# Optimization experiments

Measured on AMD Instinct MI355X. Metric: run time of the kernel, lower is better.

## Reference

```python
import jax, jax.numpy as jnp
import numpy as np


def setup_inputs() -> dict:
    key = jax.random.key(0)
    x = jax.random.normal(key, (4, 256, 64, 64), dtype=jnp.float32)
    return {"x": x}


def reference(x):
    # x: [B, C, W, H]
    B, C, W, H = x.shape
    N = W * H
    q = x.reshape(B, C, N).transpose(0, 2, 1)  # [B, N, C] (proj_query)
    # per-token L2 norm over channels
    q_norm = jnp.linalg.norm(q, ord=2, axis=2)  # [B, N]
    # outer product of norms: [B, N, N]
    nm = q_norm[:, :, None] * q_norm[:, None, :]
    # raw dot-product energy: [B, N, N]
    energy = jnp.einsum('bnc,bmc->bnm', q, q)
    norm_energy = energy / (nm + 1e-6)
    attention = jax.nn.softmax(norm_energy, axis=-1)
    return attention
```

## Files before the change

kernel.cpp:

```cpp
#include <hip/hip_runtime.h>
#include <hip/hip_bf16.h>

#define BATCH 4
#define CDIM  256
#define NTOK  4096

#define BM 64
#define BN 256

typedef short bf16x8 __attribute__((ext_vector_type(8)));
typedef float floatx4 __attribute__((ext_vector_type(4)));
typedef unsigned int uintx4 __attribute__((ext_vector_type(4)));
typedef unsigned int u32;

#define PIN(v) asm volatile("" : "+v"(v))
#define WAIT(n) asm volatile("s_waitcnt vmcnt(" #n ")" ::: "memory")
#define LGKM0() asm volatile("s_waitcnt lgkmcnt(0)" ::: "memory")
#define BAR() do { __builtin_amdgcn_s_barrier(); asm volatile("" ::: "memory"); } while (0)

__device__ inline u32 f2bf1(float f) {
    u32 u = __float_as_uint(f);
    u += 0x7fffu + ((u >> 16) & 1u);
    return u >> 16;
}
__device__ inline u32 f2bf2(float lo, float hi) { return f2bf1(lo) | (f2bf1(hi) << 16); }

__device__ inline void gload_lds16(const short* g, short* l) {
    __builtin_amdgcn_global_load_lds(
        (const __attribute__((address_space(1))) u32*)g,
        (__attribute__((address_space(3))) u32*)l, 16, 0, 0);
}

#define TT 32
__global__ __launch_bounds__(256) void prep_kernel(const float* __restrict__ x,
                                                   short* __restrict__ xn) {
    __shared__ float tile[TT][CDIM + 2];
    __shared__ float part[8][TT];
    __shared__ float rinv_s[TT];
    const int tid = threadIdx.x;
    const int blk = blockIdx.x;
    const int b = blk >> 7;
    const int t0 = (blk & 127) * TT;
    const float* xb = x + (size_t)b * CDIM * NTOK;
    const int ti = tid & 31, cq = tid >> 5;
    float ss = 0.f;
    for (int c = cq; c < CDIM; c += 8) {
        float v = xb[(size_t)c * NTOK + t0 + ti];
        tile[ti][c] = v;
        ss += v * v;
    }
    part[cq][ti] = ss;
    __syncthreads();
    if (tid < TT) {
        float s = 0.f;
#pragma unroll
        for (int q = 0; q < 8; ++q) s += part[q][tid];
        rinv_s[tid] = 1.0f / sqrtf(s);
    }
    __syncthreads();
    const int tok = tid >> 3, seg = tid & 7;
    const float ri = rinv_s[tok];
    size_t obase = ((size_t)(b * NTOK + t0 + tok)) * CDIM + seg * 32;
#pragma unroll
    for (int j = 0; j < 4; ++j) {
        u32 w[4];
#pragma unroll
        for (int u = 0; u < 4; ++u) {
            float f0 = tile[tok][seg * 32 + j * 8 + 2 * u] * ri;
            float f1 = tile[tok][seg * 32 + j * 8 + 2 * u + 1] * ri;
            w[u] = f2bf2(f0, f1);
        }
        *(uintx4*)&xn[obase + j * 8] = (uintx4){w[0], w[1], w[2], w[3]};
    }
}

__global__ __launch_bounds__(512, 2) void attn_kernel(const short* __restrict__ xn,
                                                      float* __restrict__ out) {
    __shared__ short Bs[4][256][64];
    __shared__ float rowsumLds[BM][8];
    const int tid = threadIdx.x;
    const int D = blockIdx.x;
    const int L = ((D & 7) << 5) + (D >> 3);
    const int b = L >> 6;
    const int rb = (L & 63) * BM;
    const short* xnb = xn + (size_t)b * NTOK * CDIM;
    float* outb = out + ((size_t)b << 24);
    const int lane = tid & 63, wid = tid >> 6;
    const int wcol = wid << 5;
    const int r0 = lane & 15, kq = lane >> 4;
    const int sx = r0 & 7;
    const int tr0 = wcol + r0, tr1 = wcol + 16 + r0;

    const int trl = (wid << 3) + (lane >> 3);
    const int c8 = (lane & 7) ^ (lane >> 3);

    bf16x8 afr[4][8];
#pragma unroll
    for (int m = 0; m < 4; ++m) {
        const short* arow = xnb + (size_t)(rb + m * 16 + r0) * CDIM;
#pragma unroll
        for (int j = 0; j < 8; ++j) {
            afr[m][j] = *(const bf16x8*)(arow + j * 32 + kq * 8);
            PIN(afr[m][j]);
        }
    }

    float psum[16];
#pragma unroll
    for (int i = 0; i < 16; ++i) psum[i] = 0.f;
    floatx4 acc[4][2];
    bf16x8 nb00, nb10, nb01, nb11;

    auto stage = [&](int ct, int kc) {
        const short* s0 = xnb + (size_t)(ct * BN + trl) * CDIM + kc * 64 + c8 * 8;
        short* d = &Bs[kc][wid << 3][0];
#pragma unroll
        for (int rr = 0; rr < 4; ++rr)
            gload_lds16(s0 + (size_t)(rr * 64) * CDIM, d + rr * 64 * 64);
    };

#define ACCZERO() do { _Pragma("unroll") for (int m = 0; m < 4; ++m) { \
        acc[m][0] = (floatx4){0,0,0,0}; acc[m][1] = (floatx4){0,0,0,0}; } } while (0)

#define DSREAD(KC) do { \
    const int p0 = kq ^ sx, p1 = (4 | kq) ^ sx; \
    nb00 = *(const bf16x8*)&Bs[KC][tr0][p0 * 8]; \
    nb10 = *(const bf16x8*)&Bs[KC][tr1][p0 * 8]; \
    nb01 = *(const bf16x8*)&Bs[KC][tr0][p1 * 8]; \
    nb11 = *(const bf16x8*)&Bs[KC][tr1][p1 * 8]; \
} while (0)

#define MFMA16(KC) do { \
    LGKM0(); \
    __builtin_amdgcn_sched_barrier(0); \
    __builtin_amdgcn_s_setprio(1); \
    _Pragma("unroll") for (int m = 0; m < 4; ++m) \
        acc[m][0] = __builtin_amdgcn_mfma_f32_16x16x32_bf16(afr[m][(KC)*2], nb00, acc[m][0], 0,0,0); \
    _Pragma("unroll") for (int m = 0; m < 4; ++m) \
        acc[m][1] = __builtin_amdgcn_mfma_f32_16x16x32_bf16(afr[m][(KC)*2], nb10, acc[m][1], 0,0,0); \
    _Pragma("unroll") for (int m = 0; m < 4; ++m) \
        acc[m][0] = __builtin_amdgcn_mfma_f32_16x16x32_bf16(afr[m][(KC)*2+1], nb01, acc[m][0], 0,0,0); \
    _Pragma("unroll") for (int m = 0; m < 4; ++m) \
        acc[m][1] = __builtin_amdgcn_mfma_f32_16x16x32_bf16(afr[m][(KC)*2+1], nb11, acc[m][1], 0,0,0); \
    __builtin_amdgcn_s_setprio(0); \
} while (0)

#define EPI0() do { \
    _Pragma("unroll") for (int m = 0; m < 4; ++m) \
    _Pragma("unroll") for (int r = 0; r < 4; ++r) \
        psum[m * 4 + r] += __expf(acc[m][0][r] - 1.f) + __expf(acc[m][1][r] - 1.f); \
} while (0)

#define EPI1(CT) do { \
    _Pragma("unroll") for (int m = 0; m < 4; ++m) \
    _Pragma("unroll") for (int r = 0; r < 4; ++r) { \
        const int row = rb + m * 16 + kq * 4 + r; \
        float* p = outb + ((size_t)row << 12) + ((CT) << 8) + wcol + r0; \
        const float ri = psum[m * 4 + r]; \
        __builtin_nontemporal_store(__expf(acc[m][0][r] - 1.f) * ri, p); \
        __builtin_nontemporal_store(__expf(acc[m][1][r] - 1.f) * ri, p + 16); } \
} while (0)

    stage(0, 0); stage(0, 1);
    WAIT(4); BAR();
    DSREAD(0); stage(0, 2);
    WAIT(4); BAR();
    ACCZERO();
    for (int ct = 0; ct < 15; ++ct) {
        MFMA16(0); stage(ct, 3);     WAIT(4); DSREAD(1); BAR();
        MFMA16(1); stage(ct + 1, 0); WAIT(4); DSREAD(2); BAR();
        MFMA16(2); stage(ct + 1, 1); WAIT(4); DSREAD(3); BAR();
        MFMA16(3); EPI0(); ACCZERO(); stage(ct + 1, 2); WAIT(4); DSREAD(0); BAR();
    }
    MFMA16(0); stage(15, 3); WAIT(4); DSREAD(1); BAR();
    MFMA16(1); WAIT(0); DSREAD(2); BAR();
    MFMA16(2); DSREAD(3); BAR();
    MFMA16(3); EPI0();

#pragma unroll
    for (int m = 0; m < 4; ++m)
#pragma unroll
        for (int r = 0; r < 4; ++r) {
            float v = psum[m * 4 + r];
            v += __shfl_xor(v, 1); v += __shfl_xor(v, 2);
            v += __shfl_xor(v, 4); v += __shfl_xor(v, 8);
            if (r0 == 0) rowsumLds[m * 16 + kq * 4 + r][wid] = v;
        }
    __syncthreads();
#pragma unroll
    for (int m = 0; m < 4; ++m)
#pragma unroll
        for (int r = 0; r < 4; ++r) {
            const int row = m * 16 + kq * 4 + r;
            float s = 0.f;
#pragma unroll
            for (int w = 0; w < 8; ++w) s += rowsumLds[row][w];
            psum[m * 4 + r] = 1.0f / s;
        }
    __syncthreads();

    stage(0, 0); stage(0, 1);
    WAIT(4); BAR();
    DSREAD(0); stage(0, 2);
    WAIT(4); BAR();
    ACCZERO();
    {
        MFMA16(0); stage(0, 3); WAIT(4); DSREAD(1); BAR();
        MFMA16(1); stage(1, 0); WAIT(4); DSREAD(2); BAR();
        MFMA16(2); stage(1, 1); WAIT(4); DSREAD(3); BAR();
        MFMA16(3); stage(1, 2); EPI1(0); ACCZERO(); WAIT(36); DSREAD(0); BAR();
    }
    for (int ct = 1; ct < 15; ++ct) {
        MFMA16(0); stage(ct, 3);     WAIT(36); DSREAD(1); BAR();
        MFMA16(1); stage(ct + 1, 0); WAIT(4);  DSREAD(2); BAR();
        MFMA16(2); stage(ct + 1, 1); WAIT(4);  DSREAD(3); BAR();
        MFMA16(3); stage(ct + 1, 2); EPI1(ct); ACCZERO(); WAIT(36); DSREAD(0); BAR();
    }
    MFMA16(0); stage(15, 3); WAIT(36); DSREAD(1); BAR();
    MFMA16(1); WAIT(0); DSREAD(2); BAR();
    MFMA16(2); DSREAD(3); BAR();
    MFMA16(3); EPI1(15);

#undef ACCZERO
#undef DSREAD
#undef MFMA16
#undef EPI0
#undef EPI1
}

extern "C" void kernel_launch(void* const* d_in, const int* in_sizes, int n_in,
                              void* d_out, int out_size, void* d_ws, size_t ws_size,
                              hipStream_t stream) {
    const float* x = (const float*)d_in[0];
    float* out = (float*)d_out;
    short* xn = (short*)d_ws;

    prep_kernel<<<BATCH * (NTOK / TT), 256, 0, stream>>>(x, xn);
    attn_kernel<<<NTOK / BM * BATCH, 512, 0, stream>>>(xn, out);
}
```

Before: 155.7 us.

## Split attention block across 16 waves with 2x8 warp grid

Doubles the attention kernel's block to 1024 threads and arranges the 16 waves as a 2x8 grid, so each wave now covers 32 rows instead of 64. This halves per-wave A fragments, accumulators and MFMA count, and halves per-thread staging loads. The wait counts are retuned to match, and in the second pass the epilogue stores move after the next LDS read. The aim is more waves per block to hide latency and lower register pressure. In exchange, B-tile reuse per wave drops (the MFMA-to-LDS-read ratio halves) and block-wide barriers now synchronize twice as many waves.

```diff
diff --git a/kernel.cpp b/kernel.cpp
--- a/kernel.cpp
+++ b/kernel.cpp
@@ -74,8 +74,8 @@
     }
 }
 
-__global__ __launch_bounds__(512, 2) void attn_kernel(const short* __restrict__ xn,
-                                                      float* __restrict__ out) {
+__global__ __launch_bounds__(1024) void attn_kernel(const short* __restrict__ xn,
+                                                    float* __restrict__ out) {
     __shared__ short Bs[4][256][64];
     __shared__ float rowsumLds[BM][8];
     const int tid = threadIdx.x;
@@ -86,18 +86,19 @@
     const short* xnb = xn + (size_t)b * NTOK * CDIM;
     float* outb = out + ((size_t)b << 24);
     const int lane = tid & 63, wid = tid >> 6;
-    const int wcol = wid << 5;
+    const int wr = (wid >> 3) << 5;
+    const int wcol = (wid & 7) << 5;
     const int r0 = lane & 15, kq = lane >> 4;
     const int sx = r0 & 7;
     const int tr0 = wcol + r0, tr1 = wcol + 16 + r0;
 
-    const int trl = (wid << 3) + (lane >> 3);
-    const int c8 = (lane & 7) ^ (lane >> 3);
-
-    bf16x8 afr[4][8];
-#pragma unroll
-    for (int m = 0; m < 4; ++m) {
-        const short* arow = xnb + (size_t)(rb + m * 16 + r0) * CDIM;
+    const int trl = tid >> 3;
+    const int c8 = (tid & 7) ^ (trl & 7);
+
+    bf16x8 afr[2][8];
+#pragma unroll
+    for (int m = 0; m < 2; ++m) {
+        const short* arow = xnb + (size_t)(rb + wr + m * 16 + r0) * CDIM;
 #pragma unroll
         for (int j = 0; j < 8; ++j) {
             afr[m][j] = *(const bf16x8*)(arow + j * 32 + kq * 8);
@@ -105,21 +106,20 @@
         }
     }
 
-    float psum[16];
-#pragma unroll
-    for (int i = 0; i < 16; ++i) psum[i] = 0.f;
-    floatx4 acc[4][2];
+    float psum[8];
+#pragma unroll
+    for (int i = 0; i < 8; ++i) psum[i] = 0.f;
+    floatx4 acc[2][2];
     bf16x8 nb00, nb10, nb01, nb11;
 
     auto stage = [&](int ct, int kc) {
         const short* s0 = xnb + (size_t)(ct * BN + trl) * CDIM + kc * 64 + c8 * 8;
         short* d = &Bs[kc][wid << 3][0];
-#pragma unroll
-        for (int rr = 0; rr < 4; ++rr)
-            gload_lds16(s0 + (size_t)(rr * 64) * CDIM, d + rr * 64 * 64);
+        gload_lds16(s0, d);
+        gload_lds16(s0 + (size_t)128 * CDIM, d + 128 * 64);
     };
 
-#define ACCZERO() do { _Pragma("unroll") for (int m = 0; m < 4; ++m) { \
+#define ACCZERO() do { _Pragma("unroll") for (int m = 0; m < 2; ++m) { \
         acc[m][0] = (floatx4){0,0,0,0}; acc[m][1] = (floatx4){0,0,0,0}; } } while (0)
 
 #define DSREAD(KC) do { \
@@ -130,31 +130,31 @@
     nb11 = *(const bf16x8*)&Bs[KC][tr1][p1 * 8]; \
 } while (0)
 
-#define MFMA16(KC) do { \
+#define MFMA8(KC) do { \
     LGKM0(); \
     __builtin_amdgcn_sched_barrier(0); \
     __builtin_amdgcn_s_setprio(1); \
-    _Pragma("unroll") for (int m = 0; m < 4; ++m) \
-        acc[m][0] = __builtin_amdgcn_mfma_f32_16x16x32_bf16(afr[m][(KC)*2], nb00, acc[m][0], 0,0,0); \
-    _Pragma("unroll") for (int m = 0; m < 4; ++m) \
-        acc[m][1] = __builtin_amdgcn_mfma_f32_16x16x32_bf16(afr[m][(KC)*2], nb10, acc[m][1], 0,0,0); \
-    _Pragma("unroll") for (int m = 0; m < 4; ++m) \
-        acc[m][0] = __builtin_amdgcn_mfma_f32_16x16x32_bf16(afr[m][(KC)*2+1], nb01, acc[m][0], 0,0,0); \
-    _Pragma("unroll") for (int m = 0; m < 4; ++m) \
-        acc[m][1] = __builtin_amdgcn_mfma_f32_16x16x32_bf16(afr[m][(KC)*2+1], nb11, acc[m][1], 0,0,0); \
+    acc[0][0] = __builtin_amdgcn_mfma_f32_16x16x32_bf16(afr[0][(KC)*2], nb00, acc[0][0], 0,0,0); \
+    acc[1][0] = __builtin_amdgcn_mfma_f32_16x16x32_bf16(afr[1][(KC)*2], nb00, acc[1][0], 0,0,0); \
+    acc[0][1] = __builtin_amdgcn_mfma_f32_16x16x32_bf16(afr[0][(KC)*2], nb10, acc[0][1], 0,0,0); \
+    acc[1][1] = __builtin_amdgcn_mfma_f32_16x16x32_bf16(afr[1][(KC)*2], nb10, acc[1][1], 0,0,0); \
+    acc[0][0] = __builtin_amdgcn_mfma_f32_16x16x32_bf16(afr[0][(KC)*2+1], nb01, acc[0][0], 0,0,0); \
+    acc[1][0] = __builtin_amdgcn_mfma_f32_16x16x32_bf16(afr[1][(KC)*2+1], nb01, acc[1][0], 0,0,0); \
+    acc[0][1] = __builtin_amdgcn_mfma_f32_16x16x32_bf16(afr[0][(KC)*2+1], nb11, acc[0][1], 0,0,0); \
+    acc[1][1] = __builtin_amdgcn_mfma_f32_16x16x32_bf16(afr[1][(KC)*2+1], nb11, acc[1][1], 0,0,0); \
     __builtin_amdgcn_s_setprio(0); \
 } while (0)
 
 #define EPI0() do { \
-    _Pragma("unroll") for (int m = 0; m < 4; ++m) \
+    _Pragma("unroll") for (int m = 0; m < 2; ++m) \
     _Pragma("unroll") for (int r = 0; r < 4; ++r) \
         psum[m * 4 + r] += __expf(acc[m][0][r] - 1.f) + __expf(acc[m][1][r] - 1.f); \
 } while (0)
 
 #define EPI1(CT) do { \
-    _Pragma("unroll") for (int m = 0; m < 4; ++m) \
+    _Pragma("unroll") for (int m = 0; m < 2; ++m) \
     _Pragma("unroll") for (int r = 0; r < 4; ++r) { \
-        const int row = rb + m * 16 + kq * 4 + r; \
+        const int row = rb + wr + m * 16 + kq * 4 + r; \
         float* p = outb + ((size_t)row << 12) + ((CT) << 8) + wcol + r0; \
         const float ri = psum[m * 4 + r]; \
         __builtin_nontemporal_store(__expf(acc[m][0][r] - 1.f) * ri, p); \
@@ -162,36 +162,36 @@
 } while (0)
 
     stage(0, 0); stage(0, 1);
-    WAIT(4); BAR();
+    WAIT(2); BAR();
     DSREAD(0); stage(0, 2);
-    WAIT(4); BAR();
+    WAIT(2); BAR();
     ACCZERO();
     for (int ct = 0; ct < 15; ++ct) {
-        MFMA16(0); stage(ct, 3);     WAIT(4); DSREAD(1); BAR();
-        MFMA16(1); stage(ct + 1, 0); WAIT(4); DSREAD(2); BAR();
-        MFMA16(2); stage(ct + 1, 1); WAIT(4); DSREAD(3); BAR();
-        MFMA16(3); EPI0(); ACCZERO(); stage(ct + 1, 2); WAIT(4); DSREAD(0); BAR();
-    }
-    MFMA16(0); stage(15, 3); WAIT(4); DSREAD(1); BAR();
-    MFMA16(1); WAIT(0); DSREAD(2); BAR();
-    MFMA16(2); DSREAD(3); BAR();
-    MFMA16(3); EPI0();
-
-#pragma unroll
-    for (int m = 0; m < 4; ++m)
+        MFMA8(0); stage(ct, 3);     WAIT(2); DSREAD(1); BAR();
+        MFMA8(1); stage(ct + 1, 0); WAIT(2); DSREAD(2); BAR();
+        MFMA8(2); stage(ct + 1, 1); WAIT(2); DSREAD(3); BAR();
+        MFMA8(3); EPI0(); ACCZERO(); stage(ct + 1, 2); WAIT(2); DSREAD(0); BAR();
+    }
+    MFMA8(0); stage(15, 3); WAIT(2); DSREAD(1); BAR();
+    MFMA8(1); WAIT(0); DSREAD(2); BAR();
+    MFMA8(2); DSREAD(3); BAR();
+    MFMA8(3); EPI0();
+
+#pragma unroll
+    for (int m = 0; m < 2; ++m)
 #pragma unroll
         for (int r = 0; r < 4; ++r) {
             float v = psum[m * 4 + r];
             v += __shfl_xor(v, 1); v += __shfl_xor(v, 2);
             v += __shfl_xor(v, 4); v += __shfl_xor(v, 8);
-            if (r0 == 0) rowsumLds[m * 16 + kq * 4 + r][wid] = v;
-        }
-    __syncthreads();
-#pragma unroll
-    for (int m = 0; m < 4; ++m)
+            if (r0 == 0) rowsumLds[wr + m * 16 + kq * 4 + r][wid & 7] = v;
+        }
+    __syncthreads();
+#pragma unroll
+    for (int m = 0; m < 2; ++m)
 #pragma unroll
         for (int r = 0; r < 4; ++r) {
-            const int row = m * 16 + kq * 4 + r;
+            const int row = wr + m * 16 + kq * 4 + r;
             float s = 0.f;
 #pragma unroll
             for (int w = 0; w < 8; ++w) s += rowsumLds[row][w];
@@ -200,30 +200,30 @@
     __syncthreads();
 
     stage(0, 0); stage(0, 1);
-    WAIT(4); BAR();
+    WAIT(2); BAR();
     DSREAD(0); stage(0, 2);
-    WAIT(4); BAR();
+    WAIT(2); BAR();
     ACCZERO();
     {
-        MFMA16(0); stage(0, 3); WAIT(4); DSREAD(1); BAR();
-        MFMA16(1); stage(1, 0); WAIT(4); DSREAD(2); BAR();
-        MFMA16(2); stage(1, 1); WAIT(4); DSREAD(3); BAR();
-        MFMA16(3); stage(1, 2); EPI1(0); ACCZERO(); WAIT(36); DSREAD(0); BAR();
+        MFMA8(0); stage(0, 3); WAIT(2); DSREAD(1); BAR();
+        MFMA8(1); stage(1, 0); WAIT(2); DSREAD(2); BAR();
+        MFMA8(2); stage(1, 1); WAIT(2); DSREAD(3); BAR();
+        MFMA8(3); stage(1, 2); WAIT(2); DSREAD(0); EPI1(0); ACCZERO(); BAR();
     }
     for (int ct = 1; ct < 15; ++ct) {
-        MFMA16(0); stage(ct, 3);     WAIT(36); DSREAD(1); BAR();
-        MFMA16(1); stage(ct + 1, 0); WAIT(4);  DSREAD(2); BAR();
-        MFMA16(2); stage(ct + 1, 1); WAIT(4);  DSREAD(3); BAR();
-        MFMA16(3); stage(ct + 1, 2); EPI1(ct); ACCZERO(); WAIT(36); DSREAD(0); BAR();
-    }
-    MFMA16(0); stage(15, 3); WAIT(36); DSREAD(1); BAR();
-    MFMA16(1); WAIT(0); DSREAD(2); BAR();
-    MFMA16(2); DSREAD(3); BAR();
-    MFMA16(3); EPI1(15);
+        MFMA8(0); stage(ct, 3);     WAIT(18); DSREAD(1); BAR();
+        MFMA8(1); stage(ct + 1, 0); WAIT(2);  DSREAD(2); BAR();
+        MFMA8(2); stage(ct + 1, 1); WAIT(2);  DSREAD(3); BAR();
+        MFMA8(3); stage(ct + 1, 2); WAIT(2);  DSREAD(0); EPI1(ct); ACCZERO(); BAR();
+    }
+    MFMA8(0); stage(15, 3); WAIT(18); DSREAD(1); BAR();
+    MFMA8(1); WAIT(0); DSREAD(2); BAR();
+    MFMA8(2); DSREAD(3); BAR();
+    MFMA8(3); EPI1(15);
 
 #undef ACCZERO
 #undef DSREAD
-#undef MFMA16
+#undef MFMA8
 #undef EPI0
 #undef EPI1
 }
@@ -236,5 +236,5 @@
     short* xn = (short*)d_ws;
 
     prep_kernel<<<BATCH * (NTOK / TT), 256, 0, stream>>>(x, xn);
-    attn_kernel<<<NTOK / BM * BATCH, 512, 0, stream>>>(xn, out);
-}
+    attn_kernel<<<NTOK / BM * BATCH, 1024, 0, stream>>>(xn, out);
+}
```

Result: no change. 155.2 us (-0.3%).
